# Kernel tuning notes

Measured on AMD Instinct MI355X. Metric: run time of the kernel, lower is better.

Reference implementation:

```python
import jax, jax.numpy as jnp
import numpy as np

POINT_SIZE = 1000000
LOC_DIM = 16
TIM_DIM = 16
POS_DIM = 32
INPUT_DIM = 5
HID = 32
EPS = 1e-5


def _linear(x, W, b):
    return x @ W.T + b


def _resnet(x, W1, b1, W2, b2):
    # Sequential(ReLU, Linear, ReLU, Linear, Dropout(eval=identity)); out = x + 0.3*net(x)
    h = jax.nn.relu(x)
    h = _linear(h, W1, b1)
    h = jax.nn.relu(h)
    h = _linear(h, W2, b2)
    return x + 0.3 * h


def _chain(x, rW1, rb1, rW2, rb2, W, b):
    for i in range(2):  # two ResNet blocks (fixed, structural)
        x = _resnet(x, rW1[i], rb1[i], rW2[i], rb2[i])
    return _linear(x, W, b)


def _mk_linear(key, out_dim, in_dim):
    k1, k2 = jax.random.split(key)
    s = 1.0 / np.sqrt(in_dim)
    W = jax.random.uniform(k1, (out_dim, in_dim), jnp.float32, -s, s)
    b = jax.random.uniform(k2, (out_dim,), jnp.float32, -s, s)
    return W, b


def _mk_res_stack(key, dim, n=2):
    ks = jax.random.split(key, 4 * n)
    W1s, b1s, W2s, b2s = [], [], [], []
    for i in range(n):
        W1, b1 = _mk_linear(ks[4 * i], dim, dim)
        W2, b2 = _mk_linear(ks[4 * i + 1], dim, dim)
        W1s.append(W1); b1s.append(b1); W2s.append(W2); b2s.append(b2)
    return jnp.stack(W1s), jnp.stack(b1s), jnp.stack(W2s), jnp.stack(b2s)


def setup_inputs() -> dict:
    key = jax.random.key(0)
    ks = iter(jax.random.split(key, 40))
    d = {}
    d["x"] = jax.random.randint(next(ks), (3,), 0, 24, dtype=jnp.int64 if jax.config.jax_enable_x64 else jnp.int32)
    d["hidden"] = jnp.zeros((1, 1, HID), jnp.float32)
    d["pos"] = 3
    # embeddings
    d["loc_emb"] = jax.random.normal(next(ks), (POINT_SIZE, LOC_DIM), jnp.float32)
    d["arr_emb"] = jax.random.normal(next(ks), (24, TIM_DIM), jnp.float32)
    d["dur_emb"] = jax.random.normal(next(ks), (24, TIM_DIM), jnp.float32)
    d["pos_emb"] = jax.random.normal(next(ks), (10, POS_DIM), jnp.float32)
    for name, dim in (("fc1", LOC_DIM), ("fc2", TIM_DIM), ("fc3", TIM_DIM)):
        rW1, rb1, rW2, rb2 = _mk_res_stack(next(ks), dim)
        W, b = _mk_linear(next(ks), INPUT_DIM, dim)
        d[f"{name}_rW1"], d[f"{name}_rb1"], d[f"{name}_rW2"], d[f"{name}_rb2"] = rW1, rb1, rW2, rb2
        d[f"{name}_W"], d[f"{name}_b"] = W, b
    # LayerNorm(15)
    d["ln_g"] = jnp.ones((3 * INPUT_DIM,), jnp.float32)
    d["ln_b"] = jnp.zeros((3 * INPUT_DIM,), jnp.float32)
    # ODE: Linear(5->32) + ResNet(32)
    d["ode_W"], d["ode_b"] = _mk_linear(next(ks), HID, INPUT_DIM)
    oW1, ob1, oW2, ob2 = _mk_res_stack(next(ks), HID, n=1)
    d["ode_rW1"], d["ode_rb1"], d["ode_rW2"], d["ode_rb2"] = oW1[0], ob1[0], oW2[0], ob2[0]
    # heads
    d["fc4_W"], d["fc4_b"] = _mk_linear(next(ks), POINT_SIZE, HID)
    d["fc5_W"], d["fc5_b"] = _mk_linear(next(ks), 24, HID)
    d["fc6_W"], d["fc6_b"] = _mk_linear(next(ks), 24, HID)
    # GRU (input 15, hidden 32)
    d["gru_Wih"], d["gru_bih"] = _mk_linear(next(ks), 3 * HID, 3 * INPUT_DIM)
    d["gru_Whh"], d["gru_bhh"] = _mk_linear(next(ks), 3 * HID, HID)
    return d


def reference(x, hidden, pos, loc_emb, arr_emb, dur_emb, pos_emb,
              fc1_rW1, fc1_rb1, fc1_rW2, fc1_rb2, fc1_W, fc1_b,
              fc2_rW1, fc2_rb1, fc2_rW2, fc2_rb2, fc2_W, fc2_b,
              fc3_rW1, fc3_rb1, fc3_rW2, fc3_rb2, fc3_W, fc3_b,
              ln_g, ln_b, ode_W, ode_b, ode_rW1, ode_rb1, ode_rW2, ode_rb2,
              fc4_W, fc4_b, fc5_W, fc5_b, fc6_W, fc6_b,
              gru_Wih, gru_bih, gru_Whh, gru_bhh):
    pos_e = pos_emb[pos]                                   # (32,)
    loc = _chain(loc_emb[x[0]], fc1_rW1, fc1_rb1, fc1_rW2, fc1_rb2, fc1_W, fc1_b)  # (5,)
    arr = _chain(arr_emb[x[1]], fc2_rW1, fc2_rb1, fc2_rW2, fc2_rb2, fc2_W, fc2_b)  # (5,)
    dur = _chain(dur_emb[x[2]], fc3_rW1, fc3_rb1, fc3_rW2, fc3_rb2, fc3_W, fc3_b)  # (5,)
    point = jnp.concatenate([loc, arr, dur])               # (15,)
    mu = jnp.mean(point)
    var = jnp.mean((point - mu) ** 2)
    point = (point - mu) * jax.lax.rsqrt(var + EPS) * ln_g + ln_b
    # hidden = hidden + ODE(dur)
    ode = _linear(dur, ode_W, ode_b)
    ode = _resnet(ode, ode_rW1, ode_rb1, ode_rW2, ode_rb2)
    h = hidden.reshape(-1) + ode                           # (32,)
    # single GRU step
    gi = gru_Wih @ point + gru_bih
    gh = gru_Whh @ h + gru_bhh
    i_r, i_z, i_n = jnp.split(gi, 3)
    h_r, h_z, h_n = jnp.split(gh, 3)
    r = jax.nn.sigmoid(i_r + h_r)
    z = jax.nn.sigmoid(i_z + h_z)
    n = jnp.tanh(i_n + r * h_n)
    h_new = (1.0 - z) * n + z * h                          # (32,) == out == new hidden
    next_loc = jax.nn.log_softmax(h_new @ fc4_W.T + fc4_b)
    next_arr = jax.nn.log_softmax((h_new + pos_e) @ fc5_W.T + fc5_b)
    next_dur = jax.nn.log_softmax(h_new @ fc6_W.T + fc6_b)
    return (next_loc, next_arr, next_dur, h_new.reshape(1, 1, HID))
```

## Files before the change

kernel.cpp:

```cpp
#include <hip/hip_runtime.h>
#include <math.h>
#include <float.h>

#define ROWS 1000000
#define NTHR 256
#define NBLK_L 3907
#define NBLK_B 977
#define NEG_BIG (-3.0e38f)

__global__ __launch_bounds__(128) void front_kernel(
    const int* __restrict__ x, const float* __restrict__ hidden, const int* __restrict__ pos,
    const float* __restrict__ loc_emb, const float* __restrict__ arr_emb,
    const float* __restrict__ dur_emb, const float* __restrict__ pos_emb,
    const float* __restrict__ f1rW1, const float* __restrict__ f1rb1,
    const float* __restrict__ f1rW2, const float* __restrict__ f1rb2,
    const float* __restrict__ f1W,   const float* __restrict__ f1b,
    const float* __restrict__ f2rW1, const float* __restrict__ f2rb1,
    const float* __restrict__ f2rW2, const float* __restrict__ f2rb2,
    const float* __restrict__ f2W,   const float* __restrict__ f2b,
    const float* __restrict__ f3rW1, const float* __restrict__ f3rb1,
    const float* __restrict__ f3rW2, const float* __restrict__ f3rb2,
    const float* __restrict__ f3W,   const float* __restrict__ f3b,
    const float* __restrict__ ln_g,  const float* __restrict__ ln_b,
    const float* __restrict__ ode_W, const float* __restrict__ ode_b,
    const float* __restrict__ oW1,   const float* __restrict__ ob1,
    const float* __restrict__ oW2,   const float* __restrict__ ob2,
    const float* __restrict__ fc5_W, const float* __restrict__ fc5_b,
    const float* __restrict__ fc6_W, const float* __restrict__ fc6_b,
    const float* __restrict__ gWih,  const float* __restrict__ gbih,
    const float* __restrict__ gWhh,  const float* __restrict__ gbhh,
    float* __restrict__ out, float* __restrict__ ws)
{
    __shared__ float e[3][16], tr[3][16], h1[3][16];
    __shared__ float praw[15], pnorm[15];
    __shared__ float ode0[32], odt[32], hvec[32], hnew[32], pe[32];
    __shared__ float gi[96], gh[96];
    __shared__ float a5[24], a6[24];
    __shared__ float red[4];

    const int t = threadIdx.x;

    if (t < 48) {
        int c = t >> 4, j = t & 15;
        const float* emb = (c == 0) ? (loc_emb + (size_t)x[0] * 16)
                         : (c == 1) ? (arr_emb + (size_t)x[1] * 16)
                                    : (dur_emb + (size_t)x[2] * 16);
        e[c][j] = emb[j];
    }
    if (t < 32) pe[t] = pos_emb[pos[0] * 32 + t];
    __syncthreads();

    for (int i = 0; i < 2; ++i) {
        if (t < 48) { int c = t >> 4, j = t & 15; tr[c][j] = fmaxf(e[c][j], 0.f); }
        __syncthreads();
        if (t < 48) {
            int c = t >> 4, j = t & 15;
            const float* W1 = ((c == 0) ? f1rW1 : (c == 1) ? f2rW1 : f3rW1) + i * 256 + j * 16;
            const float* b1 = ((c == 0) ? f1rb1 : (c == 1) ? f2rb1 : f3rb1) + i * 16;
            float a = b1[j];
            #pragma unroll
            for (int k = 0; k < 16; ++k) a += W1[k] * tr[c][k];
            h1[c][j] = fmaxf(a, 0.f);
        }
        __syncthreads();
        if (t < 48) {
            int c = t >> 4, j = t & 15;
            const float* W2 = ((c == 0) ? f1rW2 : (c == 1) ? f2rW2 : f3rW2) + i * 256 + j * 16;
            const float* b2 = ((c == 0) ? f1rb2 : (c == 1) ? f2rb2 : f3rb2) + i * 16;
            float a = b2[j];
            #pragma unroll
            for (int k = 0; k < 16; ++k) a += W2[k] * h1[c][k];
            e[c][j] += 0.3f * a;
        }
        __syncthreads();
    }

    if (t < 15) {
        int c = t / 5, q = t % 5;
        const float* W = ((c == 0) ? f1W : (c == 1) ? f2W : f3W) + q * 16;
        const float* b = ((c == 0) ? f1b : (c == 1) ? f2b : f3b);
        float a = b[q];
        #pragma unroll
        for (int k = 0; k < 16; ++k) a += W[k] * e[c][k];
        praw[t] = a;
    }
    __syncthreads();

    if (t == 0) {
        float mu = 0.f;
        for (int k = 0; k < 15; ++k) mu += praw[k];
        mu *= (1.f / 15.f);
        float var = 0.f;
        for (int k = 0; k < 15; ++k) { float d = praw[k] - mu; var += d * d; }
        var *= (1.f / 15.f);
        red[0] = mu;
        red[1] = rsqrtf(var + 1e-5f);
    }
    __syncthreads();
    if (t < 15) pnorm[t] = (praw[t] - red[0]) * red[1] * ln_g[t] + ln_b[t];
    if (t < 32) {
        float a = ode_b[t];
        const float* W = ode_W + t * 5;
        #pragma unroll
        for (int k = 0; k < 5; ++k) a += W[k] * praw[10 + k];
        ode0[t] = a;
    }
    __syncthreads();
    if (t < 32) {
        float a = ob1[t];
        const float* W = oW1 + t * 32;
        #pragma unroll
        for (int k = 0; k < 32; ++k) a += W[k] * fmaxf(ode0[k], 0.f);
        odt[t] = fmaxf(a, 0.f);
    }
    __syncthreads();
    if (t < 32) {
        float a = ob2[t];
        const float* W = oW2 + t * 32;
        #pragma unroll
        for (int k = 0; k < 32; ++k) a += W[k] * odt[k];
        hvec[t] = hidden[t] + ode0[t] + 0.3f * a;
    }
    __syncthreads();
    if (t < 96) {
        float a = gbih[t];
        const float* W = gWih + t * 15;
        #pragma unroll
        for (int k = 0; k < 15; ++k) a += W[k] * pnorm[k];
        gi[t] = a;
        float c2 = gbhh[t];
        const float* V = gWhh + t * 32;
        #pragma unroll
        for (int k = 0; k < 32; ++k) c2 += V[k] * hvec[k];
        gh[t] = c2;
    }
    __syncthreads();
    if (t < 32) {
        float r = 1.f / (1.f + expf(-(gi[t] + gh[t])));
        float z = 1.f / (1.f + expf(-(gi[32 + t] + gh[32 + t])));
        float n = tanhf(gi[64 + t] + r * gh[64 + t]);
        float hn = (1.f - z) * n + z * hvec[t];
        hnew[t] = hn;
        ws[t] = hn;
        out[ROWS + 48 + t] = hn;
    }
    __syncthreads();
    if (t < 24) {
        float a = fc5_b[t];
        const float* W = fc5_W + t * 32;
        #pragma unroll
        for (int k = 0; k < 32; ++k) a += W[k] * (hnew[k] + pe[k]);
        a5[t] = a;
        float b = fc6_b[t];
        const float* V = fc6_W + t * 32;
        #pragma unroll
        for (int k = 0; k < 32; ++k) b += V[k] * hnew[k];
        a6[t] = b;
    }
    __syncthreads();
    if (t == 0) {
        float m = -INFINITY;
        for (int k = 0; k < 24; ++k) m = fmaxf(m, a5[k]);
        float s = 0.f;
        for (int k = 0; k < 24; ++k) s += expf(a5[k] - m);
        red[2] = m + logf(s);
        m = -INFINITY;
        for (int k = 0; k < 24; ++k) m = fmaxf(m, a6[k]);
        s = 0.f;
        for (int k = 0; k < 24; ++k) s += expf(a6[k] - m);
        red[3] = m + logf(s);
    }
    __syncthreads();
    if (t < 24) {
        out[ROWS + t]      = a5[t] - red[2];
        out[ROWS + 24 + t] = a6[t] - red[3];
    }
}

__global__ __launch_bounds__(NTHR) void logits_kernel(
    const float* __restrict__ W, const float* __restrict__ b,
    const float* __restrict__ ws_h, float* __restrict__ out,
    float2* __restrict__ partials)
{
    __shared__ float hs[32];
    if (threadIdx.x < 32) hs[threadIdx.x] = ws_h[threadIdx.x];
    __syncthreads();

    const int t = threadIdx.x;
    const int r = blockIdx.x * NTHR + t;

    float m = NEG_BIG, s = 0.f;
    if (r < ROWS) {
        const float4* W4 = (const float4*)W;
        float4 w[8];
        #pragma unroll
        for (int j = 0; j < 8; ++j) w[j] = W4[(size_t)r * 8 + j];
        float acc = b[r];
        #pragma unroll
        for (int j = 0; j < 8; ++j)
            acc += w[j].x * hs[4*j] + w[j].y * hs[4*j+1]
                 + w[j].z * hs[4*j+2] + w[j].w * hs[4*j+3];
        out[r] = acc;
        m = acc; s = 1.f;
    }

    __shared__ float sm[NTHR], ss[NTHR];
    sm[t] = m; ss[t] = s;
    __syncthreads();
    for (int off = NTHR / 2; off > 0; off >>= 1) {
        if (t < off) {
            float m2 = sm[t + off], s2 = ss[t + off];
            float M  = fmaxf(sm[t], m2);
            ss[t] = ss[t] * __expf(sm[t] - M) + s2 * __expf(m2 - M);
            sm[t] = M;
        }
        __syncthreads();
    }
    if (t == 0) partials[blockIdx.x] = make_float2(sm[0], ss[0]);
}

__global__ __launch_bounds__(256) void finalize_kernel(
    const float2* __restrict__ partials, float* __restrict__ out)
{
    __shared__ float sm[256], ss[256];
    __shared__ float lse_sh;
    const int t = threadIdx.x;

    float fm = NEG_BIG, fs = 0.f;
    for (int i = t; i < NBLK_L; i += 256) {
        float2 p2 = partials[i];
        float M = fmaxf(fm, p2.x);
        fs = fs * __expf(fm - M) + p2.y * __expf(p2.x - M);
        fm = M;
    }
    sm[t] = fm; ss[t] = fs;
    __syncthreads();
    for (int off = 128; off > 0; off >>= 1) {
        if (t < off) {
            float m2 = sm[t + off], s2 = ss[t + off];
            float M  = fmaxf(sm[t], m2);
            ss[t] = ss[t] * __expf(sm[t] - M) + s2 * __expf(m2 - M);
            sm[t] = M;
        }
        __syncthreads();
    }
    if (t == 0) lse_sh = sm[0] + logf(ss[0]);
    __syncthreads();
    const float lse = lse_sh;

    const int idx = blockIdx.x * 256 + t;
    if (idx < ROWS / 4) {
        float4* o4 = (float4*)out;
        float4 v = o4[idx];
        v.x -= lse; v.y -= lse; v.z -= lse; v.w -= lse;
        o4[idx] = v;
    }
}

extern "C" void kernel_launch(void* const* d_in, const int* in_sizes, int n_in,
                              void* d_out, int out_size, void* d_ws, size_t ws_size,
                              hipStream_t stream) {
    const int*   x       = (const int*)  d_in[0];
    const float* hidden  = (const float*)d_in[1];
    const int*   pos     = (const int*)  d_in[2];
    const float* loc_emb = (const float*)d_in[3];
    const float* arr_emb = (const float*)d_in[4];
    const float* dur_emb = (const float*)d_in[5];
    const float* pos_emb = (const float*)d_in[6];
    const float* f1rW1 = (const float*)d_in[7];
    const float* f1rb1 = (const float*)d_in[8];
    const float* f1rW2 = (const float*)d_in[9];
    const float* f1rb2 = (const float*)d_in[10];
    const float* f1W   = (const float*)d_in[11];
    const float* f1b   = (const float*)d_in[12];
    const float* f2rW1 = (const float*)d_in[13];
    const float* f2rb1 = (const float*)d_in[14];
    const float* f2rW2 = (const float*)d_in[15];
    const float* f2rb2 = (const float*)d_in[16];
    const float* f2W   = (const float*)d_in[17];
    const float* f2b   = (const float*)d_in[18];
    const float* f3rW1 = (const float*)d_in[19];
    const float* f3rb1 = (const float*)d_in[20];
    const float* f3rW2 = (const float*)d_in[21];
    const float* f3rb2 = (const float*)d_in[22];
    const float* f3W   = (const float*)d_in[23];
    const float* f3b   = (const float*)d_in[24];
    const float* ln_g  = (const float*)d_in[25];
    const float* ln_b  = (const float*)d_in[26];
    const float* ode_W = (const float*)d_in[27];
    const float* ode_b = (const float*)d_in[28];
    const float* oW1   = (const float*)d_in[29];
    const float* ob1   = (const float*)d_in[30];
    const float* oW2   = (const float*)d_in[31];
    const float* ob2   = (const float*)d_in[32];
    const float* fc4_W = (const float*)d_in[33];
    const float* fc4_b = (const float*)d_in[34];
    const float* fc5_W = (const float*)d_in[35];
    const float* fc5_b = (const float*)d_in[36];
    const float* fc6_W = (const float*)d_in[37];
    const float* fc6_b = (const float*)d_in[38];
    const float* gWih  = (const float*)d_in[39];
    const float* gbih  = (const float*)d_in[40];
    const float* gWhh  = (const float*)d_in[41];
    const float* gbhh  = (const float*)d_in[42];

    float* out = (float*)d_out;
    float* wsf = (float*)d_ws;
    float*  ws_h        = wsf;
    float2* ws_partials = (float2*)(wsf + 64);

    front_kernel<<<1, 128, 0, stream>>>(
        x, hidden, pos, loc_emb, arr_emb, dur_emb, pos_emb,
        f1rW1, f1rb1, f1rW2, f1rb2, f1W, f1b,
        f2rW1, f2rb1, f2rW2, f2rb2, f2W, f2b,
        f3rW1, f3rb1, f3rW2, f3rb2, f3W, f3b,
        ln_g, ln_b, ode_W, ode_b, oW1, ob1, oW2, ob2,
        fc5_W, fc5_b, fc6_W, fc6_b, gWih, gbih, gWhh, gbhh,
        out, ws_h);

    logits_kernel<<<NBLK_L, NTHR, 0, stream>>>(
        fc4_W, fc4_b, ws_h, out, ws_partials);

    finalize_kernel<<<NBLK_B, 256, 0, stream>>>(ws_partials, out);
}
```

Before: 45.15 us.

## Prefetch front-kernel weights with extra warps; use wave-shuffle softmax reductions

The single-block front kernel now launches 256 threads. The extra 128 threads touch one element per 64-byte line of every small weight tensor, so later dependent reads in the serial chain find the data already in cache. The logits and finalize kernels replace their shared-memory tree reductions, which needed eight barriers each, with 64-lane shuffle merges of (max, sum) plus a four-entry cross-wave combine. The cost is extra memory traffic and threads in the front kernel, and slightly different floating-point combine order.

Measured after the change: 51.09 us. 1.13x slower.

```diff
diff --git a/kernel.cpp b/kernel.cpp
--- a/kernel.cpp
+++ b/kernel.cpp
@@ -8,7 +8,13 @@
 #define NBLK_B 977
 #define NEG_BIG (-3.0e38f)
 
-__global__ __launch_bounds__(128) void front_kernel(
+__device__ __forceinline__ float warmS(const float* p, int n, int wt) {
+    float a = 0.f;
+    for (int i = wt * 16; i < n; i += 128 * 16) a += p[i];
+    return a;
+}
+
+__global__ __launch_bounds__(256) void front_kernel(
     const int* __restrict__ x, const float* __restrict__ hidden, const int* __restrict__ pos,
     const float* __restrict__ loc_emb, const float* __restrict__ arr_emb,
     const float* __restrict__ dur_emb, const float* __restrict__ pos_emb,
@@ -40,6 +46,29 @@
 
     const int t = threadIdx.x;
 
+    if (t >= 128) {
+        const int wt = t - 128;
+        float a = warmS(gWih, 1440, wt) + warmS(gbih, 96, wt)
+                + warmS(gWhh, 3072, wt) + warmS(gbhh, 96, wt)
+                + warmS(oW1, 1024, wt)  + warmS(ob1, 32, wt)
+                + warmS(oW2, 1024, wt)  + warmS(ob2, 32, wt)
+                + warmS(ode_W, 160, wt) + warmS(ode_b, 32, wt)
+                + warmS(fc5_W, 768, wt) + warmS(fc5_b, 24, wt)
+                + warmS(fc6_W, 768, wt) + warmS(fc6_b, 24, wt)
+                + warmS(f1rW1, 512, wt) + warmS(f1rb1, 32, wt)
+                + warmS(f1rW2, 512, wt) + warmS(f1rb2, 32, wt)
+                + warmS(f2rW1, 512, wt) + warmS(f2rb1, 32, wt)
+                + warmS(f2rW2, 512, wt) + warmS(f2rb2, 32, wt)
+                + warmS(f3rW1, 512, wt) + warmS(f3rb1, 32, wt)
+                + warmS(f3rW2, 512, wt) + warmS(f3rb2, 32, wt)
+                + warmS(f1W, 80, wt) + warmS(f1b, 5, wt)
+                + warmS(f2W, 80, wt) + warmS(f2b, 5, wt)
+                + warmS(f3W, 80, wt) + warmS(f3b, 5, wt)
+                + warmS(ln_g, 15, wt) + warmS(ln_b, 15, wt)
+                + warmS(pos_emb, 320, wt) + warmS(hidden, 32, wt);
+        asm volatile("" :: "v"(a));
+    }
+
     if (t < 48) {
         int c = t >> 4, j = t & 15;
         const float* emb = (c == 0) ? (loc_emb + (size_t)x[0] * 16)
@@ -177,12 +206,24 @@
     }
 }
 
+__device__ __forceinline__ void wave_merge(float& m, float& s) {
+    #pragma unroll
+    for (int off = 1; off < 64; off <<= 1) {
+        float m2 = __shfl_xor(m, off);
+        float s2 = __shfl_xor(s, off);
+        float M  = fmaxf(m, m2);
+        s = s * __expf(m - M) + s2 * __expf(m2 - M);
+        m = M;
+    }
+}
+
 __global__ __launch_bounds__(NTHR) void logits_kernel(
     const float* __restrict__ W, const float* __restrict__ b,
     const float* __restrict__ ws_h, float* __restrict__ out,
     float2* __restrict__ partials)
 {
     __shared__ float hs[32];
+    __shared__ float2 wred[4];
     if (threadIdx.x < 32) hs[threadIdx.x] = ws_h[threadIdx.x];
     __syncthreads();
 
@@ -204,25 +245,26 @@
         m = acc; s = 1.f;
     }
 
-    __shared__ float sm[NTHR], ss[NTHR];
-    sm[t] = m; ss[t] = s;
-    __syncthreads();
-    for (int off = NTHR / 2; off > 0; off >>= 1) {
-        if (t < off) {
-            float m2 = sm[t + off], s2 = ss[t + off];
-            float M  = fmaxf(sm[t], m2);
-            ss[t] = ss[t] * __expf(sm[t] - M) + s2 * __expf(m2 - M);
-            sm[t] = M;
+    wave_merge(m, s);
+    if ((t & 63) == 0) wred[t >> 6] = make_float2(m, s);
+    __syncthreads();
+    if (t == 0) {
+        float fm = wred[0].x, fs = wred[0].y;
+        #pragma unroll
+        for (int i = 1; i < 4; ++i) {
+            float m2 = wred[i].x, s2 = wred[i].y;
+            float M  = fmaxf(fm, m2);
+            fs = fs * __expf(fm - M) + s2 * __expf(m2 - M);
+            fm = M;
         }
-        __syncthreads();
-    }
-    if (t == 0) partials[blockIdx.x] = make_float2(sm[0], ss[0]);
+        partials[blockIdx.x] = make_float2(fm, fs);
+    }
 }
 
 __global__ __launch_bounds__(256) void finalize_kernel(
     const float2* __restrict__ partials, float* __restrict__ out)
 {
-    __shared__ float sm[256], ss[256];
+    __shared__ float2 wred[4];
     __shared__ float lse_sh;
     const int t = threadIdx.x;
 
@@ -233,18 +275,20 @@
         fs = fs * __expf(fm - M) + p2.y * __expf(p2.x - M);
         fm = M;
     }
-    sm[t] = fm; ss[t] = fs;
-    __syncthreads();
-    for (int off = 128; off > 0; off >>= 1) {
-        if (t < off) {
-            float m2 = sm[t + off], s2 = ss[t + off];
-            float M  = fmaxf(sm[t], m2);
-            ss[t] = ss[t] * __expf(sm[t] - M) + s2 * __expf(m2 - M);
-            sm[t] = M;
+    wave_merge(fm, fs);
+    if ((t & 63) == 0) wred[t >> 6] = make_float2(fm, fs);
+    __syncthreads();
+    if (t == 0) {
+        float m = wred[0].x, s = wred[0].y;
+        #pragma unroll
+        for (int i = 1; i < 4; ++i) {
+            float m2 = wred[i].x, s2 = wred[i].y;
+            float M  = fmaxf(m, m2);
+            s = s * __expf(m - M) + s2 * __expf(m2 - M);
+            m = M;
         }
-        __syncthreads();
-    }
-    if (t == 0) lse_sh = sm[0] + logf(ss[0]);
+        lse_sh = m + logf(s);
+    }
     __syncthreads();
     const float lse = lse_sh;
 
@@ -309,7 +353,7 @@
     float*  ws_h        = wsf;
     float2* ws_partials = (float2*)(wsf + 64);
 
-    front_kernel<<<1, 128, 0, stream>>>(
+    front_kernel<<<1, 256, 0, stream>>>(
         x, hidden, pos, loc_emb, arr_emb, dur_emb, pos_emb,
         f1rW1, f1rb1, f1rW2, f1rb2, f1W, f1b,
         f2rW1, f2rb1, f2rW2, f2rb2, f2W, f2b,
```

## Fuse logits and log-softmax finalize into one persistent kernel with grid barrier

Applied to the files above, without the earlier changes.

Replaces the separate logits and finalize launches with a single 512-block kernel where each thread computes 8 rows, keeps logits in registers, and does an online max/sum. The last block to arrive (tracked by an atomic counter) combines the per-block partials and publishes the log-sum-exp through a flag that the other blocks spin on, and every block then writes the normalized outputs directly. This removes one kernel launch and the second read-modify-write pass over the 4 MB output. In exchange it relies on all 512 blocks being co-resident for the spin-wait, and the counter and flag are reset by the front kernel.

Measured after the change: 130.3 us. 189% more time.

```diff
diff --git a/kernel.cpp b/kernel.cpp
--- a/kernel.cpp
+++ b/kernel.cpp
@@ -4,8 +4,9 @@
 
 #define ROWS 1000000
 #define NTHR 256
-#define NBLK_L 3907
-#define NBLK_B 977
+#define K1_BLOCKS 512
+#define K1_TOTAL (K1_BLOCKS * NTHR)
+#define K1_ITERS 8
 #define NEG_BIG (-3.0e38f)
 
 __global__ __launch_bounds__(128) void front_kernel(
@@ -40,6 +41,13 @@
 
     const int t = threadIdx.x;
 
+    if (t == 127) {
+        __hip_atomic_store((unsigned long long*)(ws + 32), 0ull,
+                           __ATOMIC_RELEASE, __HIP_MEMORY_SCOPE_AGENT);
+        __hip_atomic_store((unsigned int*)(ws + 34), 0u,
+                           __ATOMIC_RELEASE, __HIP_MEMORY_SCOPE_AGENT);
+    }
+
     if (t < 48) {
         int c = t >> 4, j = t & 15;
         const float* emb = (c == 0) ? (loc_emb + (size_t)x[0] * 16)
@@ -180,28 +188,40 @@
 __global__ __launch_bounds__(NTHR) void logits_kernel(
     const float* __restrict__ W, const float* __restrict__ b,
     const float* __restrict__ ws_h, float* __restrict__ out,
-    float2* __restrict__ partials)
+    unsigned long long* __restrict__ partials,
+    unsigned long long* __restrict__ ctl,
+    unsigned int* __restrict__ counter)
 {
     __shared__ float hs[32];
-    if (threadIdx.x < 32) hs[threadIdx.x] = ws_h[threadIdx.x];
-    __syncthreads();
-
+    __shared__ int isLast;
+    __shared__ float lse_sh;
     const int t = threadIdx.x;
-    const int r = blockIdx.x * NTHR + t;
-
+    if (t < 32) hs[t] = ws_h[t];
+    __syncthreads();
+
+    const int gid = blockIdx.x * NTHR + t;
+    const float4* W4 = (const float4*)W;
+
+    float lg[K1_ITERS];
     float m = NEG_BIG, s = 0.f;
-    if (r < ROWS) {
-        const float4* W4 = (const float4*)W;
-        float4 w[8];
-        #pragma unroll
-        for (int j = 0; j < 8; ++j) w[j] = W4[(size_t)r * 8 + j];
-        float acc = b[r];
-        #pragma unroll
-        for (int j = 0; j < 8; ++j)
-            acc += w[j].x * hs[4*j] + w[j].y * hs[4*j+1]
-                 + w[j].z * hs[4*j+2] + w[j].w * hs[4*j+3];
-        out[r] = acc;
-        m = acc; s = 1.f;
+    #pragma unroll
+    for (int i = 0; i < K1_ITERS; ++i) {
+        const int r = gid + i * K1_TOTAL;
+        lg[i] = 0.f;
+        if (r < ROWS) {
+            float4 w[8];
+            #pragma unroll
+            for (int j = 0; j < 8; ++j) w[j] = W4[(size_t)r * 8 + j];
+            float acc = b[r];
+            #pragma unroll
+            for (int j = 0; j < 8; ++j)
+                acc += w[j].x * hs[4*j] + w[j].y * hs[4*j+1]
+                     + w[j].z * hs[4*j+2] + w[j].w * hs[4*j+3];
+            lg[i] = acc;
+            float M = fmaxf(m, acc);
+            s = s * __expf(m - M) + __expf(acc - M);
+            m = M;
+        }
     }
 
     __shared__ float sm[NTHR], ss[NTHR];
@@ -216,44 +236,68 @@
         }
         __syncthreads();
     }
-    if (t == 0) partials[blockIdx.x] = make_float2(sm[0], ss[0]);
-}
-
-__global__ __launch_bounds__(256) void finalize_kernel(
-    const float2* __restrict__ partials, float* __restrict__ out)
-{
-    __shared__ float sm[256], ss[256];
-    __shared__ float lse_sh;
-    const int t = threadIdx.x;
-
-    float fm = NEG_BIG, fs = 0.f;
-    for (int i = t; i < NBLK_L; i += 256) {
-        float2 p2 = partials[i];
-        float M = fmaxf(fm, p2.x);
-        fs = fs * __expf(fm - M) + p2.y * __expf(p2.x - M);
-        fm = M;
-    }
-    sm[t] = fm; ss[t] = fs;
-    __syncthreads();
-    for (int off = 128; off > 0; off >>= 1) {
-        if (t < off) {
-            float m2 = sm[t + off], s2 = ss[t + off];
-            float M  = fmaxf(sm[t], m2);
-            ss[t] = ss[t] * __expf(sm[t] - M) + s2 * __expf(m2 - M);
-            sm[t] = M;
-        }
-        __syncthreads();
-    }
-    if (t == 0) lse_sh = sm[0] + logf(ss[0]);
-    __syncthreads();
+
+    if (t == 0) {
+        unsigned long long pb = (unsigned long long)__float_as_uint(sm[0])
+                              | ((unsigned long long)__float_as_uint(ss[0]) << 32);
+        __hip_atomic_store(&partials[blockIdx.x], pb,
+                           __ATOMIC_RELEASE, __HIP_MEMORY_SCOPE_AGENT);
+        unsigned int old = __hip_atomic_fetch_add(counter, 1u,
+                           __ATOMIC_ACQ_REL, __HIP_MEMORY_SCOPE_AGENT);
+        isLast = (old == K1_BLOCKS - 1);
+    }
+    __syncthreads();
+
+    if (isLast) {
+        float fm = NEG_BIG, fs = 0.f;
+        for (int i = t; i < K1_BLOCKS; i += NTHR) {
+            unsigned long long pb = __hip_atomic_load(&partials[i],
+                                    __ATOMIC_ACQUIRE, __HIP_MEMORY_SCOPE_AGENT);
+            float pm = __uint_as_float((unsigned int)pb);
+            float ps = __uint_as_float((unsigned int)(pb >> 32));
+            float M = fmaxf(fm, pm);
+            fs = fs * __expf(fm - M) + ps * __expf(pm - M);
+            fm = M;
+        }
+        sm[t] = fm; ss[t] = fs;
+        __syncthreads();
+        for (int off = NTHR / 2; off > 0; off >>= 1) {
+            if (t < off) {
+                float m2 = sm[t + off], s2 = ss[t + off];
+                float M  = fmaxf(sm[t], m2);
+                ss[t] = ss[t] * __expf(sm[t] - M) + s2 * __expf(m2 - M);
+                sm[t] = M;
+            }
+            __syncthreads();
+        }
+        if (t == 0) {
+            float lse = sm[0] + logf(ss[0]);
+            lse_sh = lse;
+            unsigned long long packed = (1ull << 63)
+                                      | (unsigned long long)__float_as_uint(lse);
+            __hip_atomic_store(ctl, packed,
+                               __ATOMIC_RELEASE, __HIP_MEMORY_SCOPE_AGENT);
+        }
+        __syncthreads();
+    } else {
+        if (t == 0) {
+            unsigned long long v; int spins = 0;
+            do {
+                v = __hip_atomic_load(ctl, __ATOMIC_ACQUIRE,
+                                      __HIP_MEMORY_SCOPE_AGENT);
+                if (v >> 63) break;
+                __builtin_amdgcn_s_sleep(2);
+            } while (++spins < (1 << 24));
+            lse_sh = __uint_as_float((unsigned int)v);
+        }
+        __syncthreads();
+    }
     const float lse = lse_sh;
 
-    const int idx = blockIdx.x * 256 + t;
-    if (idx < ROWS / 4) {
-        float4* o4 = (float4*)out;
-        float4 v = o4[idx];
-        v.x -= lse; v.y -= lse; v.z -= lse; v.w -= lse;
-        o4[idx] = v;
+    #pragma unroll
+    for (int i = 0; i < K1_ITERS; ++i) {
+        const int r = gid + i * K1_TOTAL;
+        if (r < ROWS) out[r] = lg[i] - lse;
     }
 }
 
@@ -306,8 +350,10 @@
 
     float* out = (float*)d_out;
     float* wsf = (float*)d_ws;
-    float*  ws_h        = wsf;
-    float2* ws_partials = (float2*)(wsf + 64);
+    float*              ws_h        = wsf;
+    unsigned long long* ws_ctl      = (unsigned long long*)(wsf + 32);
+    unsigned int*       ws_counter  = (unsigned int*)(wsf + 34);
+    unsigned long long* ws_partials = (unsigned long long*)(wsf + 64);
 
     front_kernel<<<1, 128, 0, stream>>>(
         x, hidden, pos, loc_emb, arr_emb, dur_emb, pos_emb,
@@ -318,8 +364,6 @@
         fc5_W, fc5_b, fc6_W, fc6_b, gWih, gbih, gWhh, gbhh,
         out, ws_h);
 
-    logits_kernel<<<NBLK_L, NTHR, 0, stream>>>(
-        fc4_W, fc4_b, ws_h, out, ws_partials);
-
-    finalize_kernel<<<NBLK_B, 256, 0, stream>>>(ws_partials, out);
+    logits_kernel<<<K1_BLOCKS, NTHR, 0, stream>>>(
+        fc4_W, fc4_b, ws_h, out, ws_partials, ws_ctl, ws_counter);
 }
```

## Fuse front, logits and finalize into one cooperative kernel with grid syncs

Applied to the files above, without the earlier changes.

Replaces the three-kernel pipeline with a single cooperative launch. Block 0 computes the recurrent front part, a grid sync publishes the hidden state, then every thread computes four fc4 logits kept in registers. A second grid sync gives the global sum of exponentials before the normalized results are written once. This removes launch overheads and the second read/write pass over the 1M-element output, but it drops max-subtraction in the softmax and depends on co-residency of 1024 blocks.

After: 45.30 us. About the same (+0.3%).

```diff
diff --git a/kernel.cpp b/kernel.cpp
--- a/kernel.cpp
+++ b/kernel.cpp
@@ -1,12 +1,251 @@
 #include <hip/hip_runtime.h>
+#include <hip/hip_cooperative_groups.h>
 #include <math.h>
 #include <float.h>
 
+namespace cg = cooperative_groups;
+
 #define ROWS 1000000
 #define NTHR 256
+#define COOP_BLK 1024
+#define COOP_TOTAL (COOP_BLK * NTHR)
 #define NBLK_L 3907
 #define NBLK_B 977
 #define NEG_BIG (-3.0e38f)
+
+struct Params {
+    const int*   x; const float* hidden; const int* pos;
+    const float* loc_emb; const float* arr_emb; const float* dur_emb; const float* pos_emb;
+    const float* f1rW1; const float* f1rb1; const float* f1rW2; const float* f1rb2;
+    const float* f1W;   const float* f1b;
+    const float* f2rW1; const float* f2rb1; const float* f2rW2; const float* f2rb2;
+    const float* f2W;   const float* f2b;
+    const float* f3rW1; const float* f3rb1; const float* f3rW2; const float* f3rb2;
+    const float* f3W;   const float* f3b;
+    const float* ln_g;  const float* ln_b;
+    const float* ode_W; const float* ode_b;
+    const float* oW1;   const float* ob1; const float* oW2; const float* ob2;
+    const float* fc4_W; const float* fc4_b;
+    const float* fc5_W; const float* fc5_b;
+    const float* fc6_W; const float* fc6_b;
+    const float* gWih;  const float* gbih; const float* gWhh; const float* gbhh;
+    float* out; float* ws; float* partials;
+};
+
+__global__ __launch_bounds__(NTHR, 4) void coop_kernel(Params p)
+{
+    const int t   = threadIdx.x;
+    const int bid = blockIdx.x;
+
+    if (bid == 0) {
+        __shared__ float e[3][16], tr[3][16], h1[3][16];
+        __shared__ float praw[15], pnorm[15];
+        __shared__ float ode0[32], odt[32], hvec[32], hnew[32], pe[32];
+        __shared__ float gi[96], gh[96];
+        __shared__ float a5[24], a6[24];
+        __shared__ float red[4];
+
+        if (t < 48) {
+            int c = t >> 4, j = t & 15;
+            const float* emb = (c == 0) ? (p.loc_emb + (size_t)p.x[0] * 16)
+                             : (c == 1) ? (p.arr_emb + (size_t)p.x[1] * 16)
+                                        : (p.dur_emb + (size_t)p.x[2] * 16);
+            e[c][j] = emb[j];
+        }
+        if (t < 32) pe[t] = p.pos_emb[p.pos[0] * 32 + t];
+        __syncthreads();
+
+        for (int i = 0; i < 2; ++i) {
+            if (t < 48) { int c = t >> 4, j = t & 15; tr[c][j] = fmaxf(e[c][j], 0.f); }
+            __syncthreads();
+            if (t < 48) {
+                int c = t >> 4, j = t & 15;
+                const float* W1 = ((c == 0) ? p.f1rW1 : (c == 1) ? p.f2rW1 : p.f3rW1) + i * 256 + j * 16;
+                const float* b1 = ((c == 0) ? p.f1rb1 : (c == 1) ? p.f2rb1 : p.f3rb1) + i * 16;
+                float a = b1[j];
+                #pragma unroll
+                for (int k = 0; k < 16; ++k) a += W1[k] * tr[c][k];
+                h1[c][j] = fmaxf(a, 0.f);
+            }
+            __syncthreads();
+            if (t < 48) {
+                int c = t >> 4, j = t & 15;
+                const float* W2 = ((c == 0) ? p.f1rW2 : (c == 1) ? p.f2rW2 : p.f3rW2) + i * 256 + j * 16;
+                const float* b2 = ((c == 0) ? p.f1rb2 : (c == 1) ? p.f2rb2 : p.f3rb2) + i * 16;
+                float a = b2[j];
+                #pragma unroll
+                for (int k = 0; k < 16; ++k) a += W2[k] * h1[c][k];
+                e[c][j] += 0.3f * a;
+            }
+            __syncthreads();
+        }
+
+        if (t < 15) {
+            int c = t / 5, q = t % 5;
+            const float* Wf = ((c == 0) ? p.f1W : (c == 1) ? p.f2W : p.f3W) + q * 16;
+            const float* bf = ((c == 0) ? p.f1b : (c == 1) ? p.f2b : p.f3b);
+            float a = bf[q];
+            #pragma unroll
+            for (int k = 0; k < 16; ++k) a += Wf[k] * e[c][k];
+            praw[t] = a;
+        }
+        __syncthreads();
+
+        if (t == 0) {
+            float mu = 0.f;
+            for (int k = 0; k < 15; ++k) mu += praw[k];
+            mu *= (1.f / 15.f);
+            float var = 0.f;
+            for (int k = 0; k < 15; ++k) { float d = praw[k] - mu; var += d * d; }
+            var *= (1.f / 15.f);
+            red[0] = mu;
+            red[1] = rsqrtf(var + 1e-5f);
+        }
+        __syncthreads();
+        if (t < 15) pnorm[t] = (praw[t] - red[0]) * red[1] * p.ln_g[t] + p.ln_b[t];
+        if (t < 32) {
+            float a = p.ode_b[t];
+            const float* Wo = p.ode_W + t * 5;
+            #pragma unroll
+            for (int k = 0; k < 5; ++k) a += Wo[k] * praw[10 + k];
+            ode0[t] = a;
+        }
+        __syncthreads();
+        if (t < 32) {
+            float a = p.ob1[t];
+            const float* Wo = p.oW1 + t * 32;
+            #pragma unroll
+            for (int k = 0; k < 32; ++k) a += Wo[k] * fmaxf(ode0[k], 0.f);
+            odt[t] = fmaxf(a, 0.f);
+        }
+        __syncthreads();
+        if (t < 32) {
+            float a = p.ob2[t];
+            const float* Wo = p.oW2 + t * 32;
+            #pragma unroll
+            for (int k = 0; k < 32; ++k) a += Wo[k] * odt[k];
+            hvec[t] = p.hidden[t] + ode0[t] + 0.3f * a;
+        }
+        __syncthreads();
+        if (t < 96) {
+            float a = p.gbih[t];
+            const float* Wg = p.gWih + t * 15;
+            #pragma unroll
+            for (int k = 0; k < 15; ++k) a += Wg[k] * pnorm[k];
+            gi[t] = a;
+            float c2 = p.gbhh[t];
+            const float* V = p.gWhh + t * 32;
+            #pragma unroll
+            for (int k = 0; k < 32; ++k) c2 += V[k] * hvec[k];
+            gh[t] = c2;
+        }
+        __syncthreads();
+        if (t < 32) {
+            float r = 1.f / (1.f + expf(-(gi[t] + gh[t])));
+            float z = 1.f / (1.f + expf(-(gi[32 + t] + gh[32 + t])));
+            float n = tanhf(gi[64 + t] + r * gh[64 + t]);
+            float hn = (1.f - z) * n + z * hvec[t];
+            hnew[t] = hn;
+            p.ws[t] = hn;
+            p.out[ROWS + 48 + t] = hn;
+        }
+        __syncthreads();
+        if (t < 24) {
+            float a = p.fc5_b[t];
+            const float* Wf = p.fc5_W + t * 32;
+            #pragma unroll
+            for (int k = 0; k < 32; ++k) a += Wf[k] * (hnew[k] + pe[k]);
+            a5[t] = a;
+            float bb = p.fc6_b[t];
+            const float* V = p.fc6_W + t * 32;
+            #pragma unroll
+            for (int k = 0; k < 32; ++k) bb += V[k] * hnew[k];
+            a6[t] = bb;
+        }
+        __syncthreads();
+        if (t == 0) {
+            float m = -INFINITY;
+            for (int k = 0; k < 24; ++k) m = fmaxf(m, a5[k]);
+            float s = 0.f;
+            for (int k = 0; k < 24; ++k) s += expf(a5[k] - m);
+            red[2] = m + logf(s);
+            m = -INFINITY;
+            for (int k = 0; k < 24; ++k) m = fmaxf(m, a6[k]);
+            s = 0.f;
+            for (int k = 0; k < 24; ++k) s += expf(a6[k] - m);
+            red[3] = m + logf(s);
+        }
+        __syncthreads();
+        if (t < 24) {
+            p.out[ROWS + t]      = a5[t] - red[2];
+            p.out[ROWS + 24 + t] = a6[t] - red[3];
+        }
+    }
+
+    cg::this_grid().sync();
+
+    __shared__ float hs[32];
+    if (t < 16) {
+        unsigned long long v = __hip_atomic_load(
+            (const unsigned long long*)p.ws + t,
+            __ATOMIC_RELAXED, __HIP_MEMORY_SCOPE_AGENT);
+        hs[2 * t]     = __uint_as_float((unsigned int)v);
+        hs[2 * t + 1] = __uint_as_float((unsigned int)(v >> 32));
+    }
+    __syncthreads();
+
+    const int gid = bid * NTHR + t;
+    const float4* W4 = (const float4*)p.fc4_W;
+    float acc[4];
+    float s = 0.f;
+    #pragma unroll
+    for (int i = 0; i < 4; ++i) {
+        const int r = i * COOP_TOTAL + gid;
+        acc[i] = 0.f;
+        if (r < ROWS) {
+            float4 w[8];
+            #pragma unroll
+            for (int j = 0; j < 8; ++j) w[j] = W4[(size_t)r * 8 + j];
+            float a = p.fc4_b[r];
+            #pragma unroll
+            for (int j = 0; j < 8; ++j)
+                a += w[j].x * hs[4*j] + w[j].y * hs[4*j+1]
+                   + w[j].z * hs[4*j+2] + w[j].w * hs[4*j+3];
+            acc[i] = a;
+            s += __expf(a);
+        }
+    }
+
+    __shared__ float sm[NTHR];
+    __shared__ float lse_sh;
+    sm[t] = s;
+    __syncthreads();
+    for (int off = NTHR / 2; off > 0; off >>= 1) {
+        if (t < off) sm[t] += sm[t + off];
+        __syncthreads();
+    }
+    if (t == 0) p.partials[bid] = sm[0];
+
+    cg::this_grid().sync();
+
+    float tot = 0.f;
+    for (int i = t; i < COOP_BLK; i += NTHR) tot += p.partials[i];
+    sm[t] = tot;
+    __syncthreads();
+    for (int off = NTHR / 2; off > 0; off >>= 1) {
+        if (t < off) sm[t] += sm[t + off];
+        __syncthreads();
+    }
+    if (t == 0) lse_sh = logf(sm[0]);
+    __syncthreads();
+    const float lse = lse_sh;
+
+    #pragma unroll
+    for (int i = 0; i < 4; ++i) {
+        const int r = i * COOP_TOTAL + gid;
+        if (r < ROWS) p.out[r] = acc[i] - lse;
+    }
+}
 
 __global__ __launch_bounds__(128) void front_kernel(
     const int* __restrict__ x, const float* __restrict__ hidden, const int* __restrict__ pos,
@@ -260,66 +499,86 @@
 extern "C" void kernel_launch(void* const* d_in, const int* in_sizes, int n_in,
                               void* d_out, int out_size, void* d_ws, size_t ws_size,
                               hipStream_t stream) {
-    const int*   x       = (const int*)  d_in[0];
-    const float* hidden  = (const float*)d_in[1];
-    const int*   pos     = (const int*)  d_in[2];
-    const float* loc_emb = (const float*)d_in[3];
-    const float* arr_emb = (const float*)d_in[4];
-    const float* dur_emb = (const float*)d_in[5];
-    const float* pos_emb = (const float*)d_in[6];
-    const float* f1rW1 = (const float*)d_in[7];
-    const float* f1rb1 = (const float*)d_in[8];
-    const float* f1rW2 = (const float*)d_in[9];
-    const float* f1rb2 = (const float*)d_in[10];
-    const float* f1W   = (const float*)d_in[11];
-    const float* f1b   = (const float*)d_in[12];
-    const float* f2rW1 = (const float*)d_in[13];
-    const float* f2rb1 = (const float*)d_in[14];
-    const float* f2rW2 = (const float*)d_in[15];
-    const float* f2rb2 = (const float*)d_in[16];
-    const float* f2W   = (const float*)d_in[17];
-    const float* f2b   = (const float*)d_in[18];
-    const float* f3rW1 = (const float*)d_in[19];
-    const float* f3rb1 = (const float*)d_in[20];
-    const float* f3rW2 = (const float*)d_in[21];
-    const float* f3rb2 = (const float*)d_in[22];
-    const float* f3W   = (const float*)d_in[23];
-    const float* f3b   = (const float*)d_in[24];
-    const float* ln_g  = (const float*)d_in[25];
-    const float* ln_b  = (const float*)d_in[26];
-    const float* ode_W = (const float*)d_in[27];
-    const float* ode_b = (const float*)d_in[28];
-    const float* oW1   = (const float*)d_in[29];
-    const float* ob1   = (const float*)d_in[30];
-    const float* oW2   = (const float*)d_in[31];
-    const float* ob2   = (const float*)d_in[32];
-    const float* fc4_W = (const float*)d_in[33];
-    const float* fc4_b = (const float*)d_in[34];
-    const float* fc5_W = (const float*)d_in[35];
-    const float* fc5_b = (const float*)d_in[36];
-    const float* fc6_W = (const float*)d_in[37];
-    const float* fc6_b = (const float*)d_in[38];
-    const float* gWih  = (const float*)d_in[39];
-    const float* gbih  = (const float*)d_in[40];
-    const float* gWhh  = (const float*)d_in[41];
-    const float* gbhh  = (const float*)d_in[42];
+    Params pr;
+    pr.x       = (const int*)  d_in[0];
+    pr.hidden  = (const float*)d_in[1];
+    pr.pos     = (const int*)  d_in[2];
+    pr.loc_emb = (const float*)d_in[3];
+    pr.arr_emb = (const float*)d_in[4];
+    pr.dur_emb = (const float*)d_in[5];
+    pr.pos_emb = (const float*)d_in[6];
+    pr.f1rW1 = (const float*)d_in[7];
+    pr.f1rb1 = (const float*)d_in[8];
+    pr.f1rW2 = (const float*)d_in[9];
+    pr.f1rb2 = (const float*)d_in[10];
+    pr.f1W   = (const float*)d_in[11];
+    pr.f1b   = (const float*)d_in[12];
+    pr.f2rW1 = (const float*)d_in[13];
+    pr.f2rb1 = (const float*)d_in[14];
+    pr.f2rW2 = (const float*)d_in[15];
+    pr.f2rb2 = (const float*)d_in[16];
+    pr.f2W   = (const float*)d_in[17];
+    pr.f2b   = (const float*)d_in[18];
+    pr.f3rW1 = (const float*)d_in[19];
+    pr.f3rb1 = (const float*)d_in[20];
+    pr.f3rW2 = (const float*)d_in[21];
+    pr.f3rb2 = (const float*)d_in[22];
+    pr.f3W   = (const float*)d_in[23];
+    pr.f3b   = (const float*)d_in[24];
+    pr.ln_g  = (const float*)d_in[25];
+    pr.ln_b  = (const float*)d_in[26];
+    pr.ode_W = (const float*)d_in[27];
+    pr.ode_b = (const float*)d_in[28];
+    pr.oW1   = (const float*)d_in[29];
+    pr.ob1   = (const float*)d_in[30];
+    pr.oW2   = (const float*)d_in[31];
+    pr.ob2   = (const float*)d_in[32];
+    pr.fc4_W = (const float*)d_in[33];
+    pr.fc4_b = (const float*)d_in[34];
+    pr.fc5_W = (const float*)d_in[35];
+    pr.fc5_b = (const float*)d_in[36];
+    pr.fc6_W = (const float*)d_in[37];
+    pr.fc6_b = (const float*)d_in[38];
+    pr.gWih  = (const float*)d_in[39];
+    pr.gbih  = (const float*)d_in[40];
+    pr.gWhh  = (const float*)d_in[41];
+    pr.gbhh  = (const float*)d_in[42];
 
     float* out = (float*)d_out;
     float* wsf = (float*)d_ws;
+    pr.out      = out;
+    pr.ws       = wsf;
+    pr.partials = wsf + 64;
+
+    int occ = 0;
+    hipError_t oe = hipOccupancyMaxActiveBlocksPerMultiprocessor(
+        &occ, (const void*)coop_kernel, NTHR, 0);
+    bool use_coop = (oe == hipSuccess) && (occ >= 4);
+
+    if (use_coop) {
+        void* args[] = { &pr };
+        hipError_t e = hipLaunchCooperativeKernel(
+            (const void*)coop_kernel, dim3(COOP_BLK), dim3(NTHR),
+            args, 0, stream);
+        if (e == hipSuccess) return;
+        (void)hipGetLastError();
+    }
+
     float*  ws_h        = wsf;
     float2* ws_partials = (float2*)(wsf + 64);
 
     front_kernel<<<1, 128, 0, stream>>>(
-        x, hidden, pos, loc_emb, arr_emb, dur_emb, pos_emb,
-        f1rW1, f1rb1, f1rW2, f1rb2, f1W, f1b,
-        f2rW1, f2rb1, f2rW2, f2rb2, f2W, f2b,
-        f3rW1, f3rb1, f3rW2, f3rb2, f3W, f3b,
-        ln_g, ln_b, ode_W, ode_b, oW1, ob1, oW2, ob2,
-        fc5_W, fc5_b, fc6_W, fc6_b, gWih, gbih, gWhh, gbhh,
+        pr.x, pr.hidden, pr.pos, pr.loc_emb, pr.arr_emb, pr.dur_emb, pr.pos_emb,
+        pr.f1rW1, pr.f1rb1, pr.f1rW2, pr.f1rb2, pr.f1W, pr.f1b,
+        pr.f2rW1, pr.f2rb1, pr.f2rW2, pr.f2rb2, pr.f2W, pr.f2b,
+        pr.f3rW1, pr.f3rb1, pr.f3rW2, pr.f3rb2, pr.f3W, pr.f3b,
+        pr.ln_g, pr.ln_b, pr.ode_W, pr.ode_b, pr.oW1, pr.ob1, pr.oW2, pr.ob2,
+        pr.fc5_W, pr.fc5_b, pr.fc6_W, pr.fc6_b,
+        pr.gWih, pr.gbih, pr.gWhh, pr.gbhh,
         out, ws_h);
 
     logits_kernel<<<NBLK_L, NTHR, 0, stream>>>(
-        fc4_W, fc4_b, ws_h, out, ws_partials);
+        pr.fc4_W, pr.fc4_b, ws_h, out, ws_partials);
 
     finalize_kernel<<<NBLK_B, 256, 0, stream>>>(ws_partials, out);
 }
```
